# Kernel tuning notes

Measured on AMD Instinct MI355X. Metric: run time of the kernel, lower is better.

Reference implementation:

```python
import jax, jax.numpy as jnp
import numpy as np

EPS = 1e-6
MAX_RATIO = 1e6
CLAMP_ABS = 1e6

def _sanitize(x):
    x = jnp.nan_to_num(x, nan=0.0, posinf=CLAMP_ABS, neginf=-CLAMP_ABS)
    return jnp.clip(x, -CLAMP_ABS, CLAMP_ABS)

def setup_inputs() -> dict:
    key = jax.random.key(0)
    gaussians = jax.random.normal(key, (32, 65536, 14), dtype=jnp.float32)
    return {"gaussians": gaussians}

def reference(gaussians) -> jnp.ndarray:
    pos = gaussians[..., 0:3]                      # [B, N, 3]
    N = pos.shape[1]
    pc = pos - jnp.mean(pos, axis=1, keepdims=True)  # center per batch
    cov = jnp.einsum('bni,bnj->bij', pc, pc) / N     # [B, 3, 3]
    cov = _sanitize(cov)
    cov = 0.5 * (cov + jnp.swapaxes(cov, -1, -2))    # symmetrize
    eig = jnp.linalg.eigvalsh(cov)                   # ascending, [B, 3]
    max_e = jnp.clip(_sanitize(eig[..., -1]), EPS, None)
    min_e = jnp.clip(_sanitize(eig[..., 0]), EPS, None)
    ratio = jnp.clip(max_e / min_e, 1.0, MAX_RATIO)
    return -jnp.mean(jnp.log(ratio))
```

## Files before the change

### kernel.cpp

```cpp
#include <hip/hip_runtime.h>
#include <math.h>

#define BATCHES 32
#define NPTS 65536
#define CH 14
#define BLOCKS_PER_BATCH 32
#define THREADS 256
#define PPB (NPTS / BLOCKS_PER_BATCH)

__global__ __launch_bounds__(THREADS) void moments_kernel(
    const float* __restrict__ g, double* __restrict__ ws) {
    const int b   = blockIdx.x / BLOCKS_PER_BATCH;
    const int blk = blockIdx.x % BLOCKS_PER_BATCH;
    const size_t base_pt = (size_t)b * NPTS + (size_t)blk * PPB;

    float sx = 0.f, sy = 0.f, sz = 0.f;
    float sxx = 0.f, syy = 0.f, szz = 0.f;
    float sxy = 0.f, sxz = 0.f, syz = 0.f;

    for (int i = threadIdx.x; i < PPB; i += THREADS) {
        const float* p = g + (base_pt + (size_t)i) * CH;
        float2 xy = *(const float2*)p;
        float z = p[2];
        float x = xy.x, y = xy.y;
        sx += x;    sy += y;    sz += z;
        sxx += x*x; syy += y*y; szz += z*z;
        sxy += x*y; sxz += x*z; syz += y*z;
    }

    float vals[9] = {sx, sy, sz, sxx, syy, szz, sxy, sxz, syz};
#pragma unroll
    for (int k = 0; k < 9; ++k) {
        float v = vals[k];
#pragma unroll
        for (int off = 32; off >= 1; off >>= 1)
            v += __shfl_down(v, off, 64);
        vals[k] = v;
    }

    __shared__ float red[THREADS / 64][9];
    const int wave = threadIdx.x >> 6;
    const int lane = threadIdx.x & 63;
    if (lane == 0) {
#pragma unroll
        for (int k = 0; k < 9; ++k) red[wave][k] = vals[k];
    }
    __syncthreads();
    if (threadIdx.x == 0) {
#pragma unroll
        for (int k = 0; k < 9; ++k) {
            float s = red[0][k] + red[1][k] + red[2][k] + red[3][k];
            atomicAdd(&ws[b * 9 + k], (double)s);
        }
    }
}

__global__ __launch_bounds__(64) void finish_kernel(
    const double* __restrict__ ws, float* __restrict__ out) {
    __shared__ double logs[BATCHES];
    const int b = threadIdx.x;
    if (b < BATCHES) {
        const double* s = ws + b * 9;
        const double invN = 1.0 / (double)NPTS;
        double mx = s[0] * invN, my = s[1] * invN, mz = s[2] * invN;
        double a00 = s[3] * invN - mx * mx;
        double a11 = s[4] * invN - my * my;
        double a22 = s[5] * invN - mz * mz;
        double a01 = s[6] * invN - mx * my;
        double a02 = s[7] * invN - mx * mz;
        double a12 = s[8] * invN - my * mz;
        const double CL = 1e6;
        a00 = fmin(fmax(a00, -CL), CL); a11 = fmin(fmax(a11, -CL), CL);
        a22 = fmin(fmax(a22, -CL), CL); a01 = fmin(fmax(a01, -CL), CL);
        a02 = fmin(fmax(a02, -CL), CL); a12 = fmin(fmax(a12, -CL), CL);

        double q  = (a00 + a11 + a22) / 3.0;
        double p1 = a01 * a01 + a02 * a02 + a12 * a12;
        double b00 = a00 - q, b11 = a11 - q, b22 = a22 - q;
        double p2 = b00 * b00 + b11 * b11 + b22 * b22 + 2.0 * p1;
        double eigmax, eigmin;
        if (p2 <= 0.0) {
            eigmax = eigmin = q;
        } else {
            double p  = sqrt(p2 / 6.0);
            double ip = 1.0 / p;
            double c00 = b00 * ip, c11 = b11 * ip, c22 = b22 * ip;
            double c01 = a01 * ip, c02 = a02 * ip, c12 = a12 * ip;
            double detB = c00 * (c11 * c22 - c12 * c12)
                        - c01 * (c01 * c22 - c12 * c02)
                        + c02 * (c01 * c12 - c11 * c02);
            double r = detB * 0.5;
            r = fmin(1.0, fmax(-1.0, r));
            double phi = acos(r) / 3.0;
            eigmax = q + 2.0 * p * cos(phi);
            eigmin = q + 2.0 * p * cos(phi + 2.0943951023931953);
        }
        double maxe = fmax(fmin(eigmax, 1e6), 1e-6);
        double mine = fmax(fmin(eigmin, 1e6), 1e-6);
        double ratio = maxe / mine;
        ratio = fmin(fmax(ratio, 1.0), 1e6);
        logs[b] = log(ratio);
    }
    __syncthreads();
    if (threadIdx.x == 0) {
        double acc = 0.0;
#pragma unroll
        for (int i = 0; i < BATCHES; ++i) acc += logs[i];
        out[0] = (float)(-acc / (double)BATCHES);
    }
}

extern "C" void kernel_launch(void* const* d_in, const int* in_sizes, int n_in,
                              void* d_out, int out_size, void* d_ws, size_t ws_size,
                              hipStream_t stream) {
    const float* g = (const float*)d_in[0];
    float* out = (float*)d_out;
    double* ws = (double*)d_ws;

    hipMemsetAsync(ws, 0, BATCHES * 9 * sizeof(double), stream);

    moments_kernel<<<BATCHES * BLOCKS_PER_BATCH, THREADS, 0, stream>>>(g, ws);
    finish_kernel<<<1, 64, 0, stream>>>(ws, out);
}
```

Measured before the change: 171.7 us.

## Vectorize paired-point loads, double grid size, replace atomics with per-block partials

Each thread now handles two adjacent points per iteration, using two float4 loads plus one scalar load instead of a float2 plus scalar per point, and the loop is fully unrolled with a compile-time trip count. The grid doubles to 64 blocks per batch. Per-block sums are written to a float partials buffer and reduced in double by the finish kernel, which removes the memset and the double atomicAdds. The goal is more memory-level parallelism on a strided gather that touches only 3 of 14 floats per point. The cost is a serial 64-block sum per batch inside the single-block finish kernel.

```diff
diff --git a/kernel.cpp b/kernel.cpp
--- a/kernel.cpp
+++ b/kernel.cpp
@@ -4,28 +4,41 @@
 #define BATCHES 32
 #define NPTS 65536
 #define CH 14
-#define BLOCKS_PER_BATCH 32
+#define BLOCKS_PER_BATCH 64
+#define NBLOCKS (BATCHES * BLOCKS_PER_BATCH)
 #define THREADS 256
 #define PPB (NPTS / BLOCKS_PER_BATCH)
+#define PAIRS (PPB / 2)
+#define ITERS (PAIRS / THREADS)
 
 __global__ __launch_bounds__(THREADS) void moments_kernel(
-    const float* __restrict__ g, double* __restrict__ ws) {
-    const int b   = blockIdx.x / BLOCKS_PER_BATCH;
-    const int blk = blockIdx.x % BLOCKS_PER_BATCH;
-    const size_t base_pt = (size_t)b * NPTS + (size_t)blk * PPB;
+    const float* __restrict__ g, float* __restrict__ partials) {
+    const int b   = blockIdx.x >> 6;
+    const int blk = blockIdx.x & 63;
+    const float* pb = g + ((size_t)b * NPTS + (size_t)blk * PPB) * CH;
 
     float sx = 0.f, sy = 0.f, sz = 0.f;
     float sxx = 0.f, syy = 0.f, szz = 0.f;
     float sxy = 0.f, sxz = 0.f, syz = 0.f;
 
-    for (int i = threadIdx.x; i < PPB; i += THREADS) {
-        const float* p = g + (base_pt + (size_t)i) * CH;
-        float2 xy = *(const float2*)p;
-        float z = p[2];
-        float x = xy.x, y = xy.y;
-        sx += x;    sy += y;    sz += z;
-        sxx += x*x; syy += y*y; szz += z*z;
-        sxy += x*y; sxz += x*z; syz += y*z;
+#pragma unroll
+    for (int it = 0; it < ITERS; ++it) {
+        const int p = it * THREADS + threadIdx.x;
+        const float* q = pb + (size_t)p * (2 * CH);
+        const float4 a = *(const float4*)(q);
+        const float4 c = *(const float4*)(q + 12);
+        const float z1 = q[16];
+        const float x0 = a.x, y0 = a.y, z0 = a.z;
+        const float x1 = c.z, y1 = c.w;
+        sx += x0 + x1;
+        sy += y0 + y1;
+        sz += z0 + z1;
+        sxx += x0 * x0 + x1 * x1;
+        syy += y0 * y0 + y1 * y1;
+        szz += z0 * z0 + z1 * z1;
+        sxy += x0 * y0 + x1 * y1;
+        sxz += x0 * z0 + x1 * z1;
+        syz += y0 * z0 + y1 * z1;
     }
 
     float vals[9] = {sx, sy, sz, sxx, syy, szz, sxy, sxz, syz};
@@ -46,21 +59,24 @@
         for (int k = 0; k < 9; ++k) red[wave][k] = vals[k];
     }
     __syncthreads();
-    if (threadIdx.x == 0) {
-#pragma unroll
-        for (int k = 0; k < 9; ++k) {
-            float s = red[0][k] + red[1][k] + red[2][k] + red[3][k];
-            atomicAdd(&ws[b * 9 + k], (double)s);
-        }
+    if (threadIdx.x < 9) {
+        const int k = threadIdx.x;
+        partials[(size_t)blockIdx.x * 9 + k] =
+            red[0][k] + red[1][k] + red[2][k] + red[3][k];
     }
 }
 
 __global__ __launch_bounds__(64) void finish_kernel(
-    const double* __restrict__ ws, float* __restrict__ out) {
+    const float* __restrict__ partials, float* __restrict__ out) {
     __shared__ double logs[BATCHES];
     const int b = threadIdx.x;
     if (b < BATCHES) {
-        const double* s = ws + b * 9;
+        double s[9] = {0, 0, 0, 0, 0, 0, 0, 0, 0};
+        const float* p = partials + (size_t)b * BLOCKS_PER_BATCH * 9;
+        for (int j = 0; j < BLOCKS_PER_BATCH; ++j) {
+#pragma unroll
+            for (int k = 0; k < 9; ++k) s[k] += (double)p[j * 9 + k];
+        }
         const double invN = 1.0 / (double)NPTS;
         double mx = s[0] * invN, my = s[1] * invN, mz = s[2] * invN;
         double a00 = s[3] * invN - mx * mx;
@@ -82,8 +98,8 @@
         if (p2 <= 0.0) {
             eigmax = eigmin = q;
         } else {
-            double p  = sqrt(p2 / 6.0);
-            double ip = 1.0 / p;
+            double pp = sqrt(p2 / 6.0);
+            double ip = 1.0 / pp;
             double c00 = b00 * ip, c11 = b11 * ip, c22 = b22 * ip;
             double c01 = a01 * ip, c02 = a02 * ip, c12 = a12 * ip;
             double detB = c00 * (c11 * c22 - c12 * c12)
@@ -92,8 +108,8 @@
             double r = detB * 0.5;
             r = fmin(1.0, fmax(-1.0, r));
             double phi = acos(r) / 3.0;
-            eigmax = q + 2.0 * p * cos(phi);
-            eigmin = q + 2.0 * p * cos(phi + 2.0943951023931953);
+            eigmax = q + 2.0 * pp * cos(phi);
+            eigmin = q + 2.0 * pp * cos(phi + 2.0943951023931953);
         }
         double maxe = fmax(fmin(eigmax, 1e6), 1e-6);
         double mine = fmax(fmin(eigmin, 1e6), 1e-6);
@@ -115,10 +131,8 @@
                               hipStream_t stream) {
     const float* g = (const float*)d_in[0];
     float* out = (float*)d_out;
-    double* ws = (double*)d_ws;
+    float* partials = (float*)d_ws;
 
-    hipMemsetAsync(ws, 0, BATCHES * 9 * sizeof(double), stream);
-
-    moments_kernel<<<BATCHES * BLOCKS_PER_BATCH, THREADS, 0, stream>>>(g, ws);
-    finish_kernel<<<1, 64, 0, stream>>>(ws, out);
+    moments_kernel<<<NBLOCKS, THREADS, 0, stream>>>(g, partials);
+    finish_kernel<<<1, 64, 0, stream>>>(partials, out);
 }
```

Measured after the change: 176.9 us. +3.0%, slower.
